# Kernel optimization log

Measured on AMD Instinct MI355X. Metric: run time of the kernel, lower is better.

The kernel has to match this reference:

```python
import jax, jax.numpy as jnp
import numpy as np

N = 4096
C_IN = 256
C_OUT = 256
HEADS = 4
C_HEAD = C_OUT // HEADS
ALPHA = 0.2
NEG_FILL = -9e15


def setup_inputs() -> dict:
    key = jax.random.key(0)
    k1, k2, k3, k4 = jax.random.split(key, 4)
    node_feats = jax.random.normal(k1, (N, C_IN), dtype=jnp.float32)
    adj_matrix = jax.random.randint(k2, (1, N, N), 0, 2, dtype=jnp.int32)
    # xavier_uniform with gain=1.414
    lim_w = 1.414 * np.sqrt(6.0 / (C_IN + C_OUT))
    W = jax.random.uniform(k3, (C_OUT, C_IN), minval=-lim_w, maxval=lim_w, dtype=jnp.float32)
    b = jnp.zeros((C_OUT,), dtype=jnp.float32)
    lim_a = 1.414 * np.sqrt(6.0 / (HEADS + 2 * C_HEAD))
    a = jax.random.uniform(k4, (HEADS, 2 * C_HEAD), minval=-lim_a, maxval=lim_a, dtype=jnp.float32)
    return {"node_feats": node_feats, "adj_matrix": adj_matrix, "W": W, "b": b, "a": a}


def reference(node_feats, adj_matrix, W, b, a):
    # node_feats: [N, c_in] -> batch of 1, as in the torch 2D path
    h = (node_feats @ W.T + b).reshape(1, N, HEADS, C_HEAD)  # [1,N,H,c]
    a_src, a_dst = a[:, :C_HEAD], a[:, C_HEAD:]
    # attn logit for edge (i, j) = leakyrelu(a . [h_i, h_j])
    e_src = jnp.einsum('bnhc,hc->bnh', h, a_src)  # contribution of row node i
    e_dst = jnp.einsum('bnhc,hc->bnh', h, a_dst)  # contribution of col node j
    logits = jax.nn.leaky_relu(e_src[:, :, None, :] + e_dst[:, None, :, :], ALPHA)  # [1,N,N,H]
    mask = (adj_matrix == 1)[..., None]  # [1,N,N,1]
    attn = jnp.where(mask, logits, jnp.float32(NEG_FILL))
    probs = jax.nn.softmax(attn, axis=2)  # softmax over neighbors j
    out = jnp.einsum('bijh,bjhc->bihc', probs, h)  # [1,N,H,c]
    return out.reshape(1, N, HEADS * C_HEAD)  # concat heads
```

## Files before the change

### kernel.cpp

```cpp
#include <hip/hip_runtime.h>
#include <hip/hip_bf16.h>


#define NN 4096
#define LOG2E 1.4426950408889634f

typedef float f32x4 __attribute__((ext_vector_type(4)));
typedef int i32x4 __attribute__((ext_vector_type(4)));
typedef unsigned int u32x2 __attribute__((ext_vector_type(2)));
typedef unsigned int u32x4 __attribute__((ext_vector_type(4)));
typedef unsigned short u16x4 __attribute__((ext_vector_type(4)));
typedef unsigned short u16x8 __attribute__((ext_vector_type(8)));
typedef __bf16 bf16x8 __attribute__((ext_vector_type(8)));

__device__ __forceinline__ unsigned short f2bf_rne(float f) {
    unsigned int u = __builtin_bit_cast(unsigned int, f);
    u += 0x7fffu + ((u >> 16) & 1u);
    return (unsigned short)(u >> 16);
}

__device__ __forceinline__ bf16x8 ld_cvt8(const float* __restrict__ p) {
    f32x4 x = *(const f32x4*)p;
    f32x4 y = *(const f32x4*)(p + 4);
    u16x8 u;
    u[0] = f2bf_rne(x[0]); u[1] = f2bf_rne(x[1]); u[2] = f2bf_rne(x[2]); u[3] = f2bf_rne(x[3]);
    u[4] = f2bf_rne(y[0]); u[5] = f2bf_rne(y[1]); u[6] = f2bf_rne(y[2]); u[7] = f2bf_rne(y[3]);
    return __builtin_bit_cast(bf16x8, u);
}

__global__ __launch_bounds__(256) void k0_pack(const int* __restrict__ adj,
                                               unsigned long long* __restrict__ mw64) {
    const int wg   = (blockIdx.x * 256 + threadIdx.x) >> 6;
    const int lane = threadIdx.x & 63;
    const int* base = adj + wg * 2048 + lane;
    unsigned long long* outb = mw64 + wg * 32;

#pragma unroll
    for (int o = 0; o < 4; ++o) {
        int v0 = base[o * 512 + 0 * 64];
        int v1 = base[o * 512 + 1 * 64];
        int v2 = base[o * 512 + 2 * 64];
        int v3 = base[o * 512 + 3 * 64];
        int v4 = base[o * 512 + 4 * 64];
        int v5 = base[o * 512 + 5 * 64];
        int v6 = base[o * 512 + 6 * 64];
        int v7 = base[o * 512 + 7 * 64];
        unsigned long long b0 = __ballot(v0 & 1);
        unsigned long long b1 = __ballot(v1 & 1);
        unsigned long long b2 = __ballot(v2 & 1);
        unsigned long long b3 = __ballot(v3 & 1);
        unsigned long long b4 = __ballot(v4 & 1);
        unsigned long long b5 = __ballot(v5 & 1);
        unsigned long long b6 = __ballot(v6 & 1);
        unsigned long long b7 = __ballot(v7 & 1);
        const int s = lane & 7;
        unsigned long long sel = b0;
        sel = (s == 1) ? b1 : sel;
        sel = (s == 2) ? b2 : sel;
        sel = (s == 3) ? b3 : sel;
        sel = (s == 4) ? b4 : sel;
        sel = (s == 5) ? b5 : sel;
        sel = (s == 6) ? b6 : sel;
        sel = (s == 7) ? b7 : sel;
        if (lane < 8) outb[o * 8 + lane] = sel;
    }
}

__global__ __launch_bounds__(256) void k1_fused(const float* __restrict__ X,
                                                const float* __restrict__ W,
                                                const float* __restrict__ bias,
                                                const float* __restrict__ a,
                                                unsigned short* __restrict__ hB,
                                                float* __restrict__ esrc,
                                                float* __restrict__ edst) {
    const int lane = threadIdx.x & 63;
    const int hh   = threadIdx.x >> 6;
    const int row  = lane & 15;
    const int kg   = lane >> 4;
    const int rowbase = blockIdx.x * 16;

    f32x4 acc[4];
#pragma unroll
    for (int n = 0; n < 4; ++n) acc[n] = (f32x4)0.f;

#pragma unroll
    for (int kk = 0; kk < 8; ++kk) {
        const int kb = kk * 32 + kg * 8;
        bf16x8 a0 = ld_cvt8(X + (rowbase + row) * 256 + kb);
#pragma unroll
        for (int n = 0; n < 4; ++n) {
            bf16x8 bb = ld_cvt8(W + (hh * 64 + n * 16 + row) * 256 + kb);
            acc[n] = __builtin_amdgcn_mfma_f32_16x16x32_bf16(a0, bb, acc[n], 0, 0, 0);
        }
    }

    const int t   = rowbase >> 5;
    const int lp  = (((rowbase >> 4) & 1) * 2 + (kg >> 1)) * 16 + row;
    const int eoff = (kg & 1) * 4;
    unsigned short* hbb = hB + (hh * 128 + t) * 2048 + lp * 8 + eoff;

    float eS0 = 0.f, eS1 = 0.f, eS2 = 0.f, eS3 = 0.f;
    float eT0 = 0.f, eT1 = 0.f, eT2 = 0.f, eT3 = 0.f;
#pragma unroll
    for (int n = 0; n < 4; ++n) {
        const int col = hh * 64 + n * 16 + row;
        const float bv = bias[col];
        f32x4 hv;
        hv[0] = acc[n][0] + bv; hv[1] = acc[n][1] + bv;
        hv[2] = acc[n][2] + bv; hv[3] = acc[n][3] + bv;
        u16x4 us;
        us[0] = f2bf_rne(hv[0]); us[1] = f2bf_rne(hv[1]);
        us[2] = f2bf_rne(hv[2]); us[3] = f2bf_rne(hv[3]);
        *(u16x4*)(hbb + n * 512) = us;
        const float as_ = a[hh * 128 + n * 16 + row];
        const float ad_ = a[hh * 128 + 64 + n * 16 + row];
        eS0 += hv[0] * as_; eS1 += hv[1] * as_; eS2 += hv[2] * as_; eS3 += hv[3] * as_;
        eT0 += hv[0] * ad_; eT1 += hv[1] * ad_; eT2 += hv[2] * ad_; eT3 += hv[3] * ad_;
    }
#pragma unroll
    for (int d = 1; d < 16; d <<= 1) {
        eS0 += __shfl_xor(eS0, d); eS1 += __shfl_xor(eS1, d);
        eS2 += __shfl_xor(eS2, d); eS3 += __shfl_xor(eS3, d);
        eT0 += __shfl_xor(eT0, d); eT1 += __shfl_xor(eT1, d);
        eT2 += __shfl_xor(eT2, d); eT3 += __shfl_xor(eT3, d);
    }
    if (row == 0) {
        const int rb = hh * NN + rowbase + kg * 4;
        esrc[rb + 0] = eS0 * LOG2E; esrc[rb + 1] = eS1 * LOG2E;
        esrc[rb + 2] = eS2 * LOG2E; esrc[rb + 3] = eS3 * LOG2E;
        edst[rb + 0] = eT0 * LOG2E; edst[rb + 1] = eT1 * LOG2E;
        edst[rb + 2] = eT2 * LOG2E; edst[rb + 3] = eT3 * LOG2E;
    }
}

#define K3_MKP(AF, ES, MW) {                                                      \
    f32x4 s0v = E0 + (f32x4)(ES);                                                 \
    f32x4 s1v = E1 + (f32x4)(ES);                                                 \
    s0v = __builtin_elementwise_max(s0v, s0v * 0.2f);                             \
    s1v = __builtin_elementwise_max(s1v, s1v * 0.2f);                             \
    bf16x8 afv;                                                                   \
    afv[0] = (__bf16)__builtin_exp2f(s0v[0]);                                     \
    afv[1] = (__bf16)__builtin_exp2f(s0v[1]);                                     \
    afv[2] = (__bf16)__builtin_exp2f(s0v[2]);                                     \
    afv[3] = (__bf16)__builtin_exp2f(s0v[3]);                                     \
    afv[4] = (__bf16)__builtin_exp2f(s1v[0]);                                     \
    afv[5] = (__bf16)__builtin_exp2f(s1v[1]);                                     \
    afv[6] = (__bf16)__builtin_exp2f(s1v[2]);                                     \
    afv[7] = (__bf16)__builtin_exp2f(s1v[3]);                                     \
    u32x4 aw = __builtin_bit_cast(u32x4, afv);                                    \
    const u32x2 mk0 = mlut[((MW) >> kg8) & 15u];                                  \
    const u32x2 mk1 = mlut[(((MW) >> kg8) >> 4) & 15u];                           \
    aw[0] &= mk0[0]; aw[1] &= mk0[1];                                             \
    aw[2] &= mk1[0]; aw[3] &= mk1[1];                                             \
    AF = __builtin_bit_cast(bf16x8, aw);                                          \
}

__global__ __launch_bounds__(512, 4) void k3_flash(const unsigned int* __restrict__ mw32,
                                                   const unsigned short* __restrict__ hB,
                                                   const float* __restrict__ esrc,
                                                   const float* __restrict__ edst,
                                                   float* __restrict__ out) {
    __shared__ float lacc[8][16][64];
    __shared__ float lls[8][16];
    __shared__ u32x2 mlut[16];

    const int lane = threadIdx.x & 63;
    const int q  = threadIdx.x >> 6;
    const int hh = blockIdx.x & 3;
    const int ib = blockIdx.x >> 2;
    const int i0 = ib * 32;
    const int row = lane & 15;
    const int kg  = lane >> 4;
    const int kg8 = kg * 8;

    if (threadIdx.x < 16) {
        const unsigned n = threadIdx.x;
        u32x2 m;
        m[0] = ((n & 1u) ? 0xFFFFu : 0u) | ((n & 2u) ? 0xFFFF0000u : 0u);
        m[1] = ((n & 4u) ? 0xFFFFu : 0u) | ((n & 8u) ? 0xFFFF0000u : 0u);
        mlut[n] = m;
    }
    __syncthreads();

    const float es0 = esrc[hh * NN + i0 + row];
    const float es1 = esrc[hh * NN + i0 + 16 + row];
    const unsigned int* mwp = mw32 + (i0 + row) * 128 + q * 16;
    const float* eD = edst + hh * NN + q * 512 + kg * 8;
    const unsigned short* hBp = hB + ((hh * 128 + q * 16) * 256 + lane) * 8;

    u16x8 ou;
    const unsigned short ov = (row == 0) ? (unsigned short)0x3F80 : (unsigned short)0;
#pragma unroll
    for (int e = 0; e < 8; ++e) ou[e] = ov;
    const bf16x8 bOnes = __builtin_bit_cast(bf16x8, ou);

    f32x4 aA0 = (f32x4)0.f, aA1 = (f32x4)0.f, aA2 = (f32x4)0.f,
          aA3 = (f32x4)0.f, aA4 = (f32x4)0.f;
    f32x4 aB0 = (f32x4)0.f, aB1 = (f32x4)0.f, aB2 = (f32x4)0.f,
          aB3 = (f32x4)0.f, aB4 = (f32x4)0.f;

    for (int td = 0; td < 4; ++td) {
        const u32x4 M0 = *(const u32x4*)(mwp + td * 4);
        const u32x4 M1 = *(const u32x4*)(mwp + 16 * 128 + td * 4);
        const float* eDt = eD + td * 128;
        const unsigned short* hBt = hBp + td * 8192;
#pragma unroll
        for (int ti = 0; ti < 4; ++ti) {
            const f32x4 E0 = *(const f32x4*)(eDt + ti * 32);
            const f32x4 E1 = *(const f32x4*)(eDt + ti * 32 + 4);
            const u16x8 B0 = *(const u16x8*)(hBt + ti * 2048);
            const u16x8 B1 = *(const u16x8*)(hBt + ti * 2048 + 512);
            const u16x8 B2 = *(const u16x8*)(hBt + ti * 2048 + 1024);
            const u16x8 B3 = *(const u16x8*)(hBt + ti * 2048 + 1536);
            bf16x8 af0, af1;
            K3_MKP(af0, es0, M0[ti])
            K3_MKP(af1, es1, M1[ti])
            aA0 = __builtin_amdgcn_mfma_f32_16x16x32_bf16(af0, __builtin_bit_cast(bf16x8, B0), aA0, 0, 0, 0);
            aA1 = __builtin_amdgcn_mfma_f32_16x16x32_bf16(af0, __builtin_bit_cast(bf16x8, B1), aA1, 0, 0, 0);
            aA2 = __builtin_amdgcn_mfma_f32_16x16x32_bf16(af0, __builtin_bit_cast(bf16x8, B2), aA2, 0, 0, 0);
            aA3 = __builtin_amdgcn_mfma_f32_16x16x32_bf16(af0, __builtin_bit_cast(bf16x8, B3), aA3, 0, 0, 0);
            aA4 = __builtin_amdgcn_mfma_f32_16x16x32_bf16(af0, bOnes, aA4, 0, 0, 0);
            aB0 = __builtin_amdgcn_mfma_f32_16x16x32_bf16(af1, __builtin_bit_cast(bf16x8, B0), aB0, 0, 0, 0);
            aB1 = __builtin_amdgcn_mfma_f32_16x16x32_bf16(af1, __builtin_bit_cast(bf16x8, B1), aB1, 0, 0, 0);
            aB2 = __builtin_amdgcn_mfma_f32_16x16x32_bf16(af1, __builtin_bit_cast(bf16x8, B2), aB2, 0, 0, 0);
            aB3 = __builtin_amdgcn_mfma_f32_16x16x32_bf16(af1, __builtin_bit_cast(bf16x8, B3), aB3, 0, 0, 0);
            aB4 = __builtin_amdgcn_mfma_f32_16x16x32_bf16(af1, bOnes, aB4, 0, 0, 0);
        }
    }

#pragma unroll
    for (int n = 0; n < 4; ++n) {
        f32x4 an = (n == 0) ? aA0 : (n == 1) ? aA1 : (n == 2) ? aA2 : aA3;
#pragma unroll
        for (int r = 0; r < 4; ++r)
            lacc[q][kg * 4 + r][n * 16 + row] = an[r];
    }
    if (row == 0) {
#pragma unroll
        for (int r = 0; r < 4; ++r) lls[q][kg * 4 + r] = aA4[r];
    }
    __syncthreads();
    if (threadIdx.x < 256) {
        const int idx = threadIdx.x * 4;
        const int r2 = idx >> 6;
        const int c  = idx & 63;
        f32x4 v = (f32x4)0.f;
        float l = 0.f;
#pragma unroll
        for (int q2 = 0; q2 < 8; ++q2) {
            v += *(const f32x4*)&lacc[q2][r2][c];
            l += lls[q2][r2];
        }
        const float inv = 1.f / l;
        f32x4 o;
        o[0] = v[0] * inv; o[1] = v[1] * inv; o[2] = v[2] * inv; o[3] = v[3] * inv;
        *(f32x4*)(out + (i0 + r2) * 256 + hh * 64 + c) = o;
    }
    __syncthreads();

#pragma unroll
    for (int n = 0; n < 4; ++n) {
        f32x4 an = (n == 0) ? aB0 : (n == 1) ? aB1 : (n == 2) ? aB2 : aB3;
#pragma unroll
        for (int r = 0; r < 4; ++r)
            lacc[q][kg * 4 + r][n * 16 + row] = an[r];
    }
    if (row == 0) {
#pragma unroll
        for (int r = 0; r < 4; ++r) lls[q][kg * 4 + r] = aB4[r];
    }
    __syncthreads();
    if (threadIdx.x < 256) {
        const int idx = threadIdx.x * 4;
        const int r2 = idx >> 6;
        const int c  = idx & 63;
        f32x4 v = (f32x4)0.f;
        float l = 0.f;
#pragma unroll
        for (int q2 = 0; q2 < 8; ++q2) {
            v += *(const f32x4*)&lacc[q2][r2][c];
            l += lls[q2][r2];
        }
        const float inv = 1.f / l;
        f32x4 o;
        o[0] = v[0] * inv; o[1] = v[1] * inv; o[2] = v[2] * inv; o[3] = v[3] * inv;
        *(f32x4*)(out + (i0 + 16 + r2) * 256 + hh * 64 + c) = o;
    }
}

extern "C" void kernel_launch(void* const* d_in, const int* in_sizes, int n_in,
                              void* d_out, int out_size, void* d_ws, size_t ws_size,
                              hipStream_t stream) {
    const float* X    = (const float*)d_in[0];
    const int*   adj  = (const int*)d_in[1];
    const float* W    = (const float*)d_in[2];
    const float* bias = (const float*)d_in[3];
    const float* a    = (const float*)d_in[4];
    float* out = (float*)d_out;

    char* ws = (char*)d_ws;
    unsigned int*   mw   = (unsigned int*)(ws);
    unsigned short* hB   = (unsigned short*)(ws + (2 << 20));
    float*          esrc = (float*)(ws + (4 << 20));
    float*          edst = (float*)(ws + (4 << 20) + (64 << 10));

    k0_pack<<<2048, 256, 0, stream>>>(adj, (unsigned long long*)mw);
    k1_fused<<<256, 256, 0, stream>>>(X, W, bias, a, hB, esrc, edst);
    k3_flash<<<512, 512, 0, stream>>>(mw, hB, esrc, edst, out);
}
```

Baseline: 56.03 us.

## Stream adjacency into LDS with double-buffered direct loads in pack kernel

The adjacency bit-packing kernel now uses 16-byte global_load_lds transfers straight into per-wave LDS buffers, double-buffered across eight iterations. This replaces many scalar dword global loads. Each wave now processes 4096 elements instead of 2048, and the grid is halved to match. The goal is more bytes in flight per instruction and overlap of the loads with the ballot/pack work on the 64MB int32 mask. In exchange it relies on manual vmcnt waits, adds LDS use, and depends on the 16-byte LDS-load variant being supported.

After: 57.39 us. +2.4%, slower.

```diff
diff --git a/kernel.cpp b/kernel.cpp
--- a/kernel.cpp
+++ b/kernel.cpp
@@ -30,29 +30,45 @@
 
 __global__ __launch_bounds__(256) void k0_pack(const int* __restrict__ adj,
                                                unsigned long long* __restrict__ mw64) {
-    const int wg   = (blockIdx.x * 256 + threadIdx.x) >> 6;
+    __shared__ unsigned int abuf[4][2][512];
+
+    const int w    = threadIdx.x >> 6;
     const int lane = threadIdx.x & 63;
-    const int* base = adj + wg * 2048 + lane;
-    unsigned long long* outb = mw64 + wg * 32;
-
-#pragma unroll
-    for (int o = 0; o < 4; ++o) {
-        int v0 = base[o * 512 + 0 * 64];
-        int v1 = base[o * 512 + 1 * 64];
-        int v2 = base[o * 512 + 2 * 64];
-        int v3 = base[o * 512 + 3 * 64];
-        int v4 = base[o * 512 + 4 * 64];
-        int v5 = base[o * 512 + 5 * 64];
-        int v6 = base[o * 512 + 6 * 64];
-        int v7 = base[o * 512 + 7 * 64];
-        unsigned long long b0 = __ballot(v0 & 1);
-        unsigned long long b1 = __ballot(v1 & 1);
-        unsigned long long b2 = __ballot(v2 & 1);
-        unsigned long long b3 = __ballot(v3 & 1);
-        unsigned long long b4 = __ballot(v4 & 1);
-        unsigned long long b5 = __ballot(v5 & 1);
-        unsigned long long b6 = __ballot(v6 & 1);
-        unsigned long long b7 = __ballot(v7 & 1);
+    const long wbase = ((long)blockIdx.x * 4 + w) * 4096;
+    const unsigned int* gsrc = (const unsigned int*)adj + wbase + lane * 4;
+    unsigned long long* outw = mw64 + (wbase >> 6);
+
+#pragma unroll
+    for (int j = 0; j < 2; ++j)
+        __builtin_amdgcn_global_load_lds(
+            (const __attribute__((address_space(1))) void*)(gsrc + j * 256),
+            (__attribute__((address_space(3))) void*)(&abuf[w][0][j * 256]),
+            16, 0, 0);
+
+    for (int it = 0; it < 8; ++it) {
+        if (it < 7) {
+            const int nb = (it + 1) & 1;
+#pragma unroll
+            for (int j = 0; j < 2; ++j)
+                __builtin_amdgcn_global_load_lds(
+                    (const __attribute__((address_space(1))) void*)(gsrc + (it + 1) * 512 + j * 256),
+                    (__attribute__((address_space(3))) void*)(&abuf[w][nb][j * 256]),
+                    16, 0, 0);
+            asm volatile("s_waitcnt vmcnt(2)" ::: "memory");
+        } else {
+            asm volatile("s_waitcnt vmcnt(0)" ::: "memory");
+        }
+        __builtin_amdgcn_sched_barrier(0);
+
+        const unsigned int* ab = &abuf[w][it & 1][0];
+        unsigned long long b0 = __ballot(ab[0 * 64 + lane] & 1);
+        unsigned long long b1 = __ballot(ab[1 * 64 + lane] & 1);
+        unsigned long long b2 = __ballot(ab[2 * 64 + lane] & 1);
+        unsigned long long b3 = __ballot(ab[3 * 64 + lane] & 1);
+        unsigned long long b4 = __ballot(ab[4 * 64 + lane] & 1);
+        unsigned long long b5 = __ballot(ab[5 * 64 + lane] & 1);
+        unsigned long long b6 = __ballot(ab[6 * 64 + lane] & 1);
+        unsigned long long b7 = __ballot(ab[7 * 64 + lane] & 1);
         const int s = lane & 7;
         unsigned long long sel = b0;
         sel = (s == 1) ? b1 : sel;
@@ -62,7 +78,7 @@
         sel = (s == 5) ? b5 : sel;
         sel = (s == 6) ? b6 : sel;
         sel = (s == 7) ? b7 : sel;
-        if (lane < 8) outb[o * 8 + lane] = sel;
+        if (lane < 8) outw[it * 8 + lane] = sel;
     }
 }
 
@@ -304,7 +320,7 @@
     float*          esrc = (float*)(ws + (4 << 20));
     float*          edst = (float*)(ws + (4 << 20) + (64 << 10));
 
-    k0_pack<<<2048, 256, 0, stream>>>(adj, (unsigned long long*)mw);
+    k0_pack<<<1024, 256, 0, stream>>>(adj, (unsigned long long*)mw);
     k1_fused<<<256, 256, 0, stream>>>(X, W, bias, a, hB, esrc, edst);
     k3_flash<<<512, 512, 0, stream>>>(mw, hB, esrc, edst, out);
 }
```
